# Kernel optimization log

Hardware: AMD Instinct MI355X
Metric: run time of the kernel (lower is better)

Reference implementation:

```python
import jax, jax.numpy as jnp
import numpy as np

N_NODES = 50000
N_EDGES = 1000000
D_IN = 128
HID = 64
N_GRAPHS = 256
NEG_SLOPE = 0.2


def _gatv2_layer(x, src, dst, Wl, Wr, att, b, n_nodes):
    # lin_l applied to source nodes, lin_r to target nodes (PyG GATv2Conv, heads=1)
    xl = x @ Wl.T  # [N, C]
    xr = x @ Wr.T  # [N, C]
    e = jax.nn.leaky_relu(xl[src] + xr[dst], NEG_SLOPE)  # [E, C]
    logits = e @ att  # [E]
    # segment softmax over destination node
    m = jax.ops.segment_max(logits, dst, num_segments=n_nodes)
    ex = jnp.exp(logits - m[dst])
    den = jax.ops.segment_sum(ex, dst, num_segments=n_nodes)
    alpha = ex / den[dst]  # [E]
    out = jax.ops.segment_sum(alpha[:, None] * xl[src], dst, num_segments=n_nodes)
    return out + b


def setup_inputs() -> dict:
    key = jax.random.key(0)
    ks = jax.random.split(key, 32)
    x = jax.random.normal(ks[0], (N_NODES, D_IN), dtype=jnp.float32)
    edge_index = jax.random.randint(ks[1], (2, N_EDGES), 0, N_NODES, dtype=jnp.int64)
    batch = jnp.sort(jax.random.randint(ks[2], (N_NODES,), 0, N_GRAPHS, dtype=jnp.int64))
    inp = {"x": x, "edge_index": edge_index, "batch": batch}
    dims = [D_IN, HID, HID]  # input dim per layer
    kidx = 3
    for i, din in enumerate(dims):
        inp[f"Wl{i}"] = jax.random.normal(ks[kidx], (HID, din), dtype=jnp.float32) * 0.1; kidx += 1
        inp[f"Wr{i}"] = jax.random.normal(ks[kidx], (HID, din), dtype=jnp.float32) * 0.1; kidx += 1
        inp[f"att{i}"] = jax.random.normal(ks[kidx], (HID,), dtype=jnp.float32) * 0.1; kidx += 1
        inp[f"b{i}"] = jnp.zeros((HID,), dtype=jnp.float32)
        inp[f"Rw{i}"] = jax.random.normal(ks[kidx], (HID, din), dtype=jnp.float32) * 0.1; kidx += 1
        inp[f"Rb{i}"] = jnp.zeros((HID,), dtype=jnp.float32)
    inp["Wf"] = jax.random.normal(ks[kidx], (1, HID), dtype=jnp.float32) * 0.1
    inp["bf"] = jnp.zeros((1,), dtype=jnp.float32)
    return inp


def reference(x, edge_index, batch, Wl0, Wr0, att0, b0, Rw0, Rb0,
              Wl1, Wr1, att1, b1, Rw1, Rb1,
              Wl2, Wr2, att2, b2, Rw2, Rb2, Wf, bf):
    n = x.shape[0]
    # add_self_loops=True (PyG default)
    loops = jnp.arange(n, dtype=edge_index.dtype)
    src = jnp.concatenate([edge_index[0], loops])
    dst = jnp.concatenate([edge_index[1], loops])
    layers = [(Wl0, Wr0, att0, b0, Rw0, Rb0),
              (Wl1, Wr1, att1, b1, Rw1, Rb1),
              (Wl2, Wr2, att2, b2, Rw2, Rb2)]
    for i, (Wl, Wr, att, b, Rw, Rb) in enumerate(layers):
        h = _gatv2_layer(x, src, dst, Wl, Wr, att, b, n) + (x @ Rw.T + Rb)  # res=True
        # norm=None -> Identity; dropout inactive at inference
        x = jax.nn.relu(h) if i < len(layers) - 1 else h
    # global_mean_pool
    sums = jax.ops.segment_sum(x, batch, num_segments=N_GRAPHS)
    cnt = jax.ops.segment_sum(jnp.ones((n,), x.dtype), batch, num_segments=N_GRAPHS)
    pooled = sums / jnp.maximum(cnt, 1.0)[:, None]
    return pooled @ Wf.T + bf
```

## Files before the change

kernel.cpp:

```cpp
#include <hip/hip_runtime.h>


#define NN 50000
#define NE 1000000
#define HID 64
#define DIN0 128
#define NG 256
#define NEG 0.2f

#define SCHUNK 1024
#define SNB ((NN + SCHUNK - 1) / SCHUNK)

typedef float f32x4 __attribute__((ext_vector_type(4)));
typedef short s8v __attribute__((ext_vector_type(8)));
typedef short s4v __attribute__((ext_vector_type(4)));
typedef __bf16 bf16x8 __attribute__((ext_vector_type(8)));
typedef _Float16 h2v __attribute__((ext_vector_type(2)));
typedef unsigned u32x2 __attribute__((ext_vector_type(2)));
typedef unsigned short u16;

__device__ __forceinline__ unsigned short f2bf(float f) {
    unsigned u = __float_as_uint(f);
    u = u + 0x7fffu + ((u >> 16) & 1u);
    return (unsigned short)(u >> 16);
}
__device__ __forceinline__ float bf2f(unsigned short v) {
    return __uint_as_float(((unsigned)v) << 16);
}
__device__ __forceinline__ short split_hi(float x) {
    return (short)f2bf(x);
}
__device__ __forceinline__ short split_lo(float x, short hi) {
    return (short)f2bf(x - bf2f((unsigned short)hi));
}
__device__ __forceinline__ h2v u2h(unsigned u) { return __builtin_bit_cast(h2v, u); }
__device__ __forceinline__ unsigned h2u(h2v h) { return __builtin_bit_cast(unsigned, h); }
__device__ __forceinline__ h2v pklo(unsigned a, unsigned b) {
    return u2h(__builtin_amdgcn_perm(b, a, 0x05040100u));
}
__device__ __forceinline__ h2v pkhi(unsigned a, unsigned b) {
    return u2h(__builtin_amdgcn_perm(b, a, 0x07060302u));
}
__device__ __forceinline__ float red32_add(float v) {
    unsigned u = __float_as_uint(v);
    u32x2 r = __builtin_amdgcn_permlane32_swap(u, u, false, false);
    return __uint_as_float(r[0]) + __uint_as_float(r[1]);
}
__device__ __forceinline__ float red32_max(float v) {
    unsigned u = __float_as_uint(v);
    u32x2 r = __builtin_amdgcn_permlane32_swap(u, u, false, false);
    return fmaxf(__uint_as_float(r[0]), __uint_as_float(r[1]));
}

__global__ __launch_bounds__(256) void k_wt_all(
        const float* __restrict__ Wl0, const float* __restrict__ Wr0, const float* __restrict__ Rw0,
        const float* __restrict__ Wl1, const float* __restrict__ Wr1, const float* __restrict__ Rw1,
        const float* __restrict__ Wl2, const float* __restrict__ Wr2, const float* __restrict__ Rw2,
        const float* __restrict__ att0, const float* __restrict__ att1, const float* __restrict__ att2,
        short* __restrict__ Ws0, short* __restrict__ Ws1, short* __restrict__ Ws2,
        _Float16* __restrict__ attp,
        int* __restrict__ startg, int* __restrict__ endg) {
    int i = blockIdx.x * 256 + threadIdx.x;
    if (i < 2 * NG) {
        if (i < NG) startg[i] = 0; else endg[i - NG] = 0;
    }
    if (i < 3 * HID) {
        int L = i >> 6, c = i & 63;
        const float* at = (L == 0) ? att0 : (L == 1) ? att1 : att2;
        float a = at[c];
        attp[L * 2 * HID + c] = (_Float16)(0.6f * a);
        attp[L * 2 * HID + HID + c] = (_Float16)(0.4f * a);
    }
    const int L0N = 3 * HID * DIN0;
    const int L1N = 3 * HID * HID;
    if (i >= L0N + 2 * L1N) return;
    const float* Wm; short* Ws; int din, local;
    if (i < L0N) {
        local = i; din = DIN0; Ws = Ws0;
        int m = local / (DIN0 * HID);
        Wm = (m == 0) ? Wl0 : (m == 1) ? Wr0 : Rw0;
    } else if (i < L0N + L1N) {
        local = i - L0N; din = HID; Ws = Ws1;
        int m = local / (HID * HID);
        Wm = (m == 0) ? Wl1 : (m == 1) ? Wr1 : Rw1;
    } else {
        local = i - L0N - L1N; din = HID; Ws = Ws2;
        int m = local / (HID * HID);
        Wm = (m == 0) ? Wl2 : (m == 1) ? Wr2 : Rw2;
    }
    int m = local / (din * HID);
    int r = local - m * (din * HID);
    int c = r / din, k = r - c * din;
    float w = Wm[c * din + k];
    short hi = split_hi(w);
    short lo = split_lo(w, hi);
    Ws[(((m * 2 + 0) * HID + c) * din) + k] = hi;
    Ws[(((m * 2 + 1) * HID + c) * din) + k] = lo;
}

__global__ void k_bounds(const int* __restrict__ batch,
                         int* __restrict__ startg, int* __restrict__ endg,
                         int* __restrict__ cnt8) {
    int i = blockIdx.x * 256 + threadIdx.x;
    if (i >= NN) return;
#pragma unroll
    for (int g = 0; g < 8; g++) cnt8[g * NN + i] = 0;
    int g = batch[i];
    if (i == 0 || batch[i - 1] != g) startg[g] = i;
    if (i == NN - 1 || batch[i + 1] != g) endg[g] = i + 1;
}

__global__ __launch_bounds__(256) void k_hist8(const int* __restrict__ edst,
                                               int* __restrict__ cnt8,
                                               u16* __restrict__ rank) {
    int* mycnt = cnt8 + (blockIdx.x & 7) * NN;
    for (int e = blockIdx.x * 256 + threadIdx.x; e < NE; e += 512 * 256) {
        int r = atomicAdd(&mycnt[edst[e]], 1);
        rank[e] = (u16)r;
    }
}

__global__ void k_hist_red(int* __restrict__ cnt8, int* __restrict__ cnt) {
    int i = blockIdx.x * 256 + threadIdx.x;
    if (i >= NN) return;
    int s = 1;
#pragma unroll
    for (int g = 0; g < 8; g++) {
        int t = cnt8[g * NN + i];
        cnt8[g * NN + i] = s;
        s += t;
    }
    cnt[i] = s;
}

__global__ __launch_bounds__(256) void k_scan_part(const int* __restrict__ cnt,
                                                   int* __restrict__ part) {
    __shared__ int ws[4];
    int b = blockIdx.x, t = threadIdx.x;
    int i0 = b * SCHUNK + t * 4;
    int s = 0;
#pragma unroll
    for (int j = 0; j < 4; j++) {
        int i = i0 + j;
        if (i < NN) s += cnt[i];
    }
#pragma unroll
    for (int o = 32; o; o >>= 1) s += __shfl_xor(s, o, 64);
    if ((t & 63) == 0) ws[t >> 6] = s;
    __syncthreads();
    if (t == 0) part[b] = ws[0] + ws[1] + ws[2] + ws[3];
}

__global__ void k_scan_small(const int* __restrict__ part, int* __restrict__ partScan) {
    __shared__ int sh[SNB];
    int t = threadIdx.x;
    if (t < SNB) sh[t] = part[t];
    __syncthreads();
    if (t < SNB) {
        int s = 0;
        for (int i = 0; i < t; i++) s += sh[i];
        partScan[t] = s;
    }
}

__global__ __launch_bounds__(256) void k_scan_emit(const int* __restrict__ cnt,
                                                   const int* __restrict__ partScan,
                                                   int* __restrict__ off,
                                                   u16* __restrict__ srcs) {
    __shared__ int tsum[256];
    int b = blockIdx.x, t = threadIdx.x;
    int i0 = b * SCHUNK + t * 4;
    int e[4], p[4];
    int s = 0;
#pragma unroll
    for (int j = 0; j < 4; j++) {
        int i = i0 + j;
        e[j] = (i < NN) ? cnt[i] : 0;
        p[j] = s;
        s += e[j];
    }
    tsum[t] = s;
    __syncthreads();
    for (int d = 1; d < 256; d <<= 1) {
        int v = (t >= d) ? tsum[t - d] : 0;
        __syncthreads();
        tsum[t] += v;
        __syncthreads();
    }
    int base = partScan[b] + ((t == 0) ? 0 : tsum[t - 1]);
#pragma unroll
    for (int j = 0; j < 4; j++) {
        int i = i0 + j;
        if (i < NN) {
            int v = base + p[j];
            off[i] = v;
            srcs[v] = (u16)i;
            if (i == NN - 1) off[NN] = v + e[j];
        }
    }
}

__global__ __launch_bounds__(256) void k_scatter_rank(
        const int* __restrict__ esrc, const int* __restrict__ edst,
        const int* __restrict__ off, const int* __restrict__ cnt8,
        const u16* __restrict__ rank, u16* __restrict__ srcs) {
    int e = blockIdx.x * 256 + threadIdx.x;
    if (e >= NE) return;
    int d = edst[e];
    int slice = (e >> 8) & 7;
    int pos = off[d] + cnt8[slice * NN + d] + (int)rank[e];
    srcs[pos] = (u16)esrc[e];
}

template <int DIN, bool RELU>
__global__ __launch_bounds__(256, 3) void k_gemm(
        const float* __restrict__ xin, const short* __restrict__ Ws,
        const float* __restrict__ bvec, const float* __restrict__ rb,
        _Float16* __restrict__ xl16, _Float16* __restrict__ xr16, float* __restrict__ acc) {
    constexpr int LROW = 40;
    __shared__ short lds[20480];
    short* xhi = lds;
    short* xlo = lds + 2560;

    const int tid = threadIdx.x;
    const int w = tid >> 6;
    const int lane = tid & 63;
    const int col = lane & 15;
    const int quad = lane >> 4;
    const int nb0 = blockIdx.x * 64;

    f32x4 d[3][4];
#pragma unroll
    for (int m = 0; m < 3; m++)
#pragma unroll
        for (int ct = 0; ct < 4; ct++) d[m][ct] = (f32x4){0.f, 0.f, 0.f, 0.f};

    for (int c0 = 0; c0 < DIN; c0 += 32) {
        if (c0) __syncthreads();
        for (int u = tid; u < 512; u += 256) {
            int row = u >> 3, kq = u & 7;
            int n = nb0 + row;
            float4 v = make_float4(0.f, 0.f, 0.f, 0.f);
            if (n < NN) {
                v = *(const float4*)&xin[(size_t)n * DIN + c0 + 4 * kq];
                if (RELU) {
                    v.x = fmaxf(v.x, 0.f); v.y = fmaxf(v.y, 0.f);
                    v.z = fmaxf(v.z, 0.f); v.w = fmaxf(v.w, 0.f);
                }
            }
            s4v h, l;
            short h0 = split_hi(v.x), l0 = split_lo(v.x, h0);
            short h1 = split_hi(v.y), l1 = split_lo(v.y, h1);
            short h2 = split_hi(v.z), l2 = split_lo(v.z, h2);
            short h3 = split_hi(v.w), l3 = split_lo(v.w, h3);
            h[0] = h0; h[1] = h1; h[2] = h2; h[3] = h3;
            l[0] = l0; l[1] = l1; l[2] = l2; l[3] = l3;
            *(s4v*)&xhi[row * LROW + 4 * kq] = h;
            *(s4v*)&xlo[row * LROW + 4 * kq] = l;
        }
        for (int u = tid; u < 1536; u += 256) {
            int mp = u >> 8;
            int r = u & 255;
            int c = r >> 2, q = r & 3;
            s8v v = *(const s8v*)&Ws[((mp * HID + c) * DIN) + c0 + 8 * q];
            *(s8v*)&lds[5120 + mp * 2560 + c * LROW + 8 * q] = v;
        }
        __syncthreads();

        bf16x8 a_h = __builtin_bit_cast(bf16x8,
            *(const s8v*)&xhi[(w * 16 + col) * LROW + quad * 8]);
        bf16x8 a_l = __builtin_bit_cast(bf16x8,
            *(const s8v*)&xlo[(w * 16 + col) * LROW + quad * 8]);

#pragma unroll
        for (int m = 0; m < 3; m++) {
#pragma unroll
            for (int ct = 0; ct < 4; ct++) {
                bf16x8 b_h = __builtin_bit_cast(bf16x8,
                    *(const s8v*)&lds[5120 + (m * 2 + 0) * 2560 + (ct * 16 + col) * LROW + quad * 8]);
                bf16x8 b_l = __builtin_bit_cast(bf16x8,
                    *(const s8v*)&lds[5120 + (m * 2 + 1) * 2560 + (ct * 16 + col) * LROW + quad * 8]);
                d[m][ct] = __builtin_amdgcn_mfma_f32_16x16x32_bf16(a_h, b_h, d[m][ct], 0, 0, 0);
                d[m][ct] = __builtin_amdgcn_mfma_f32_16x16x32_bf16(a_h, b_l, d[m][ct], 0, 0, 0);
                d[m][ct] = __builtin_amdgcn_mfma_f32_16x16x32_bf16(a_l, b_h, d[m][ct], 0, 0, 0);
            }
        }
    }

#pragma unroll
    for (int r = 0; r < 4; r++) {
        int n = nb0 + w * 16 + quad * 4 + r;
        if (n >= NN) continue;
        size_t base = (size_t)n * HID;
#pragma unroll
        for (int ct = 0; ct < 4; ct++) {
            int c = ct * 16 + col;
            xl16[base + c] = (_Float16)d[0][ct][r];
            xr16[base + c] = (_Float16)d[1][ct][r];
            acc[base + c] = d[2][ct][r] + bvec[c] + rb[c];
        }
    }
}

__global__ __launch_bounds__(256) void k_attn_dst(
        const int* __restrict__ off, const u16* __restrict__ srcs,
        const _Float16* __restrict__ xl16, const _Float16* __restrict__ xr16,
        const _Float16* __restrict__ attL, float* __restrict__ acc) {
    const int lane = threadIdx.x & 63;
    const int d = blockIdx.x * 4 + (threadIdx.x >> 6);
    if (d >= NN) return;
    const int e = lane >> 3;
    const int cg = lane & 7;

    const int lo = off[d], deg = off[d + 1] - lo;

    uint4 X = *(const uint4*)&xr16[(size_t)d * HID + 8 * cg];
    uint4 A6 = *(const uint4*)&attL[8 * cg];
    uint4 A4 = *(const uint4*)&attL[HID + 8 * cg];
    h2v xh0 = u2h(X.x), xh1 = u2h(X.y), xh2 = u2h(X.z), xh3 = u2h(X.w);
    h2v a60 = u2h(A6.x), a61 = u2h(A6.y), a62 = u2h(A6.z), a63 = u2h(A6.w);
    h2v a40 = u2h(A4.x), a41 = u2h(A4.y), a42 = u2h(A4.z), a43 = u2h(A4.w);

#define EDGE_LOGIT(S, U, T)                                                    \
    {                                                                          \
        U = *(const uint4*)&xl16[(size_t)(S) * HID + 8 * cg];                  \
        h2v _v; unsigned _a; float _ps;                                        \
        _v = u2h(U.x) + xh0; _a = h2u(_v) & 0x7FFF7FFFu;                       \
        _ps = __builtin_amdgcn_fdot2(a60, _v, 0.f, false);                     \
        _ps = __builtin_amdgcn_fdot2(a40, u2h(_a), _ps, false);                \
        _v = u2h(U.y) + xh1; _a = h2u(_v) & 0x7FFF7FFFu;                       \
        _ps = __builtin_amdgcn_fdot2(a61, _v, _ps, false);                     \
        _ps = __builtin_amdgcn_fdot2(a41, u2h(_a), _ps, false);                \
        _v = u2h(U.z) + xh2; _a = h2u(_v) & 0x7FFF7FFFu;                       \
        _ps = __builtin_amdgcn_fdot2(a62, _v, _ps, false);                     \
        _ps = __builtin_amdgcn_fdot2(a42, u2h(_a), _ps, false);                \
        _v = u2h(U.w) + xh3; _a = h2u(_v) & 0x7FFF7FFFu;                       \
        _ps = __builtin_amdgcn_fdot2(a63, _v, _ps, false);                     \
        _ps = __builtin_amdgcn_fdot2(a43, u2h(_a), _ps, false);                \
        _ps += __shfl_xor(_ps, 1, 64);                                         \
        _ps += __shfl_xor(_ps, 2, 64);                                         \
        _ps += __shfl_xor(_ps, 4, 64);                                         \
        T = _ps;                                                               \
    }

    float m = -INFINITY, l = 0.f;
    float4 oA = make_float4(0.f, 0.f, 0.f, 0.f);
    float4 oB = make_float4(0.f, 0.f, 0.f, 0.f);

    for (int base = 0; base < deg; base += 32) {
        const int rem = deg - base;
        int s0 = (int)srcs[lo + min(base + e, deg - 1)];
        int s1 = (int)srcs[lo + min(base + 8 + e, deg - 1)];

        uint4 U0, U1, U2, U3;
        float t0, t1, t2 = -INFINITY, t3 = -INFINITY;
        EDGE_LOGIT(s0, U0, t0);
        EDGE_LOGIT(s1, U1, t1);
        if (base + e >= deg) t0 = -INFINITY;
        if (base + 8 + e >= deg) t1 = -INFINITY;

        const bool do2 = rem > 16;
        if (do2) {
            int s2 = (int)srcs[lo + min(base + 16 + e, deg - 1)];
            EDGE_LOGIT(s2, U2, t2);
            if (base + 16 + e >= deg) t2 = -INFINITY;
            if (rem > 24) {
                int s3 = (int)srcs[lo + min(base + 24 + e, deg - 1)];
                EDGE_LOGIT(s3, U3, t3);
                if (base + 24 + e >= deg) t3 = -INFINITY;
            } else {
                U3 = U0;
            }
        }

        float cm = fmaxf(fmaxf(t0, t1), fmaxf(t2, t3));
        cm = fmaxf(cm, __shfl_xor(cm, 8, 64));
        cm = fmaxf(cm, __shfl_xor(cm, 16, 64));
        cm = red32_max(cm);
        if (cm > m) {
            float corr = __expf(m - cm);
            m = cm;
            l *= corr;
            oA.x *= corr; oA.y *= corr; oA.z *= corr; oA.w *= corr;
            oB.x *= corr; oB.y *= corr; oB.z *= corr; oB.w *= corr;
        }
        float p0 = __expf(t0 - m);
        float p1 = __expf(t1 - m);
        l += p0 + p1;
        h2v p01 = {(_Float16)p0, (_Float16)p1};
        oA.x = __builtin_amdgcn_fdot2(p01, pklo(U0.x, U1.x), oA.x, false);
        oA.y = __builtin_amdgcn_fdot2(p01, pkhi(U0.x, U1.x), oA.y, false);
        oA.z = __builtin_amdgcn_fdot2(p01, pklo(U0.y, U1.y), oA.z, false);
        oA.w = __builtin_amdgcn_fdot2(p01, pkhi(U0.y, U1.y), oA.w, false);
        oB.x = __builtin_amdgcn_fdot2(p01, pklo(U0.z, U1.z), oB.x, false);
        oB.y = __builtin_amdgcn_fdot2(p01, pkhi(U0.z, U1.z), oB.y, false);
        oB.z = __builtin_amdgcn_fdot2(p01, pklo(U0.w, U1.w), oB.z, false);
        oB.w = __builtin_amdgcn_fdot2(p01, pkhi(U0.w, U1.w), oB.w, false);
        if (do2) {
            float p2 = __expf(t2 - m);
            float p3 = __expf(t3 - m);
            l += p2 + p3;
            h2v p23 = {(_Float16)p2, (_Float16)p3};
            oA.x = __builtin_amdgcn_fdot2(p23, pklo(U2.x, U3.x), oA.x, false);
            oA.y = __builtin_amdgcn_fdot2(p23, pkhi(U2.x, U3.x), oA.y, false);
            oA.z = __builtin_amdgcn_fdot2(p23, pklo(U2.y, U3.y), oA.z, false);
            oA.w = __builtin_amdgcn_fdot2(p23, pkhi(U2.y, U3.y), oA.w, false);
            oB.x = __builtin_amdgcn_fdot2(p23, pklo(U2.z, U3.z), oB.x, false);
            oB.y = __builtin_amdgcn_fdot2(p23, pkhi(U2.z, U3.z), oB.y, false);
            oB.z = __builtin_amdgcn_fdot2(p23, pklo(U2.w, U3.w), oB.z, false);
            oB.w = __builtin_amdgcn_fdot2(p23, pkhi(U2.w, U3.w), oB.w, false);
        }
    }
#undef EDGE_LOGIT

#pragma unroll
    for (int w = 8; w <= 16; w <<= 1) {
        l    += __shfl_xor(l, w, 64);
        oA.x += __shfl_xor(oA.x, w, 64); oA.y += __shfl_xor(oA.y, w, 64);
        oA.z += __shfl_xor(oA.z, w, 64); oA.w += __shfl_xor(oA.w, w, 64);
        oB.x += __shfl_xor(oB.x, w, 64); oB.y += __shfl_xor(oB.y, w, 64);
        oB.z += __shfl_xor(oB.z, w, 64); oB.w += __shfl_xor(oB.w, w, 64);
    }
    l    = red32_add(l);
    oA.x = red32_add(oA.x); oA.y = red32_add(oA.y);
    oA.z = red32_add(oA.z); oA.w = red32_add(oA.w);
    oB.x = red32_add(oB.x); oB.y = red32_add(oB.y);
    oB.z = red32_add(oB.z); oB.w = red32_add(oB.w);

    if (e == 0) {
        float inv = 1.f / l;
        float4* a4 = (float4*)&acc[(size_t)d * HID + 8 * cg];
        float4 c0 = a4[0], c1 = a4[1];
        c0.x += oA.x * inv; c0.y += oA.y * inv;
        c0.z += oA.z * inv; c0.w += oA.w * inv;
        c1.x += oB.x * inv; c1.y += oB.y * inv;
        c1.z += oB.z * inv; c1.w += oB.w * inv;
        a4[0] = c0; a4[1] = c1;
    }
}

__global__ __launch_bounds__(512) void k_pool_final(
        const float* __restrict__ acc,
        const int* __restrict__ startg, const int* __restrict__ endg,
        const float* __restrict__ Wf, const float* __restrict__ bf_,
        float* __restrict__ out) {
    __shared__ float red[8][HID];
    const int g = blockIdx.x;
    const int c = threadIdx.x & 63;
    const int j = threadIdx.x >> 6;
    const int s = startg[g], epos = endg[g];

    float sum = 0.f;
    for (int n = s + j; n < epos; n += 8)
        sum += acc[(size_t)n * HID + c];
    red[j][c] = sum;
    __syncthreads();

    if (threadIdx.x < HID) {
        float tot = 0.f;
#pragma unroll
        for (int w = 0; w < 8; w++) tot += red[w][c];
        float cntf = (float)(epos - s);
        float v = tot / fmaxf(cntf, 1.f) * Wf[c];
#pragma unroll
        for (int o = 32; o; o >>= 1) v += __shfl_xor(v, o, 64);
        if (c == 0) out[g] = v + bf_[0];
    }
}

extern "C" void kernel_launch(void* const* d_in, const int* in_sizes, int n_in,
                              void* d_out, int out_size, void* d_ws, size_t ws_size,
                              hipStream_t stream) {
    const float* x   = (const float*)d_in[0];
    const int* eidx  = (const int*)d_in[1];
    const int* batch = (const int*)d_in[2];
    const int* esrc = eidx;
    const int* edst = eidx + NE;
    const float* Wf  = (const float*)d_in[21];
    const float* bfb = (const float*)d_in[22];

    float* wsf = (float*)d_ws;
    const size_t NN64 = (size_t)NN * HID;
    _Float16* xl16 = (_Float16*)wsf;
    _Float16* xr16 = (_Float16*)(wsf + NN64);
    float* acc0   = wsf + 2 * NN64;
    float* acc1   = acc0 + NN64;
    short* Ws0    = (short*)(acc1 + NN64);
    short* Ws1    = Ws0 + 2 * 3 * HID * DIN0;
    short* Ws2    = Ws1 + 2 * 3 * HID * HID;
    int*   ccnt   = (int*)(Ws2 + 2 * 3 * HID * HID);
    int*   startg = ccnt + NN;
    int*   endg   = startg + NG;
    int*   off    = endg + NG;
    int*   part   = off + NN + 1;
    int*   partSc = part + SNB;
    int*   cnt8   = partSc + SNB;
    u16*   rank   = (u16*)(cnt8 + 8 * NN);
    u16*   srcs   = rank + NE;
    _Float16* attp = (_Float16*)(srcs + NE + NN);

    k_wt_all<<<(3 * HID * DIN0 + 2 * 3 * HID * HID + 255) / 256, 256, 0, stream>>>(
        (const float*)d_in[3], (const float*)d_in[4], (const float*)d_in[7],
        (const float*)d_in[9], (const float*)d_in[10], (const float*)d_in[13],
        (const float*)d_in[15], (const float*)d_in[16], (const float*)d_in[19],
        (const float*)d_in[5], (const float*)d_in[11], (const float*)d_in[17],
        Ws0, Ws1, Ws2, attp, startg, endg);
    k_bounds<<<(NN + 255) / 256, 256, 0, stream>>>(batch, startg, endg, cnt8);

    k_hist8<<<512, 256, 0, stream>>>(edst, cnt8, rank);
    k_hist_red<<<(NN + 255) / 256, 256, 0, stream>>>(cnt8, ccnt);
    k_scan_part<<<SNB, 256, 0, stream>>>(ccnt, part);
    k_scan_small<<<1, 64, 0, stream>>>(part, partSc);
    k_scan_emit<<<SNB, 256, 0, stream>>>(ccnt, partSc, off, srcs);
    k_scatter_rank<<<(NE + 255) / 256, 256, 0, stream>>>(esrc, edst, off, cnt8, rank, srcs);

    const short* Wss[3] = {Ws0, Ws1, Ws2};
    float* accs[4] = {acc0, acc0, acc1, acc0};
    const int gemm_grid = (NN + 63) / 64;
    for (int L = 0; L < 3; L++) {
        const float* b   = (const float*)d_in[3 + L * 6 + 3];
        const float* Rb  = (const float*)d_in[3 + L * 6 + 5];
        float* accOut = accs[L + 1];

        if (L == 0)
            k_gemm<DIN0, false><<<gemm_grid, 256, 0, stream>>>(
                x, Wss[0], b, Rb, xl16, xr16, accOut);
        else
            k_gemm<HID, true><<<gemm_grid, 256, 0, stream>>>(
                accs[L], Wss[L], b, Rb, xl16, xr16, accOut);

        k_attn_dst<<<(NN + 3) / 4, 256, 0, stream>>>(
            off, srcs, xl16, xr16, attp + L * 2 * HID, accOut);
    }

    k_pool_final<<<NG, 512, 0, stream>>>(accs[3], startg, endg, Wf, bfb, (float*)d_out);
}
```

Before: 347.3 us.

## Fuse preprocessing kernels and use DPP/swizzle reductions in attention

Merges weight split and batch-bounds into one prep kernel, folds the histogram reduction into the scan-partial kernel, and replaces the single-block partial scan with a per-block wave reduction, cutting three kernel launches. In the attention kernel, the octet and cross-octet reductions use DPP and ds_swizzle in place of generic shuffles, dot products use two independent accumulators, and all source indices are loaded up front. This reduces launch overhead and cross-lane reduction latency, at the cost of more register pressure and redundant source loads for low-degree nodes.

```diff
diff --git a/kernel.cpp b/kernel.cpp
--- a/kernel.cpp
+++ b/kernel.cpp
@@ -41,6 +41,15 @@
 __device__ __forceinline__ h2v pkhi(unsigned a, unsigned b) {
     return u2h(__builtin_amdgcn_perm(b, a, 0x07060302u));
 }
+template <int CTRL>
+__device__ __forceinline__ float dpp_mv(float v) {
+    return __int_as_float(
+        __builtin_amdgcn_update_dpp(0, __float_as_int(v), CTRL, 0xF, 0xF, true));
+}
+template <int OFF>
+__device__ __forceinline__ float swz(float v) {
+    return __int_as_float(__builtin_amdgcn_ds_swizzle(__float_as_int(v), OFF));
+}
 __device__ __forceinline__ float red32_add(float v) {
     unsigned u = __float_as_uint(v);
     u32x2 r = __builtin_amdgcn_permlane32_swap(u, u, false, false);
@@ -51,25 +60,58 @@
     u32x2 r = __builtin_amdgcn_permlane32_swap(u, u, false, false);
     return fmaxf(__uint_as_float(r[0]), __uint_as_float(r[1]));
 }
-
-__global__ __launch_bounds__(256) void k_wt_all(
+__device__ __forceinline__ float octet_sum(float v) {
+    v += dpp_mv<0xB1>(v);
+    v += dpp_mv<0x4E>(v);
+    v += swz<0x101F>(v);
+    return v;
+}
+__device__ __forceinline__ float esum(float v) {
+    v += dpp_mv<0x128>(v);
+    v += swz<0x401F>(v);
+    return red32_add(v);
+}
+__device__ __forceinline__ float emax(float v) {
+    v = fmaxf(v, dpp_mv<0x128>(v));
+    v = fmaxf(v, swz<0x401F>(v));
+    return red32_max(v);
+}
+
+__global__ __launch_bounds__(256) void k_prep(
         const float* __restrict__ Wl0, const float* __restrict__ Wr0, const float* __restrict__ Rw0,
         const float* __restrict__ Wl1, const float* __restrict__ Wr1, const float* __restrict__ Rw1,
         const float* __restrict__ Wl2, const float* __restrict__ Wr2, const float* __restrict__ Rw2,
         const float* __restrict__ att0, const float* __restrict__ att1, const float* __restrict__ att2,
         short* __restrict__ Ws0, short* __restrict__ Ws1, short* __restrict__ Ws2,
         _Float16* __restrict__ attp,
-        int* __restrict__ startg, int* __restrict__ endg) {
+        const int* __restrict__ batch,
+        int* __restrict__ startg, int* __restrict__ endg,
+        int* __restrict__ cnt8) {
     int i = blockIdx.x * 256 + threadIdx.x;
-    if (i < 2 * NG) {
-        if (i < NG) startg[i] = 0; else endg[i - NG] = 0;
-    }
     if (i < 3 * HID) {
         int L = i >> 6, c = i & 63;
         const float* at = (L == 0) ? att0 : (L == 1) ? att1 : att2;
         float a = at[c];
         attp[L * 2 * HID + c] = (_Float16)(0.6f * a);
         attp[L * 2 * HID + HID + c] = (_Float16)(0.4f * a);
+    }
+    if (i < NN) {
+#pragma unroll
+        for (int g = 0; g < 8; g++) cnt8[g * NN + i] = 0;
+        int g = batch[i];
+        if (i == 0) {
+            startg[g] = 0;
+            for (int g2 = 0; g2 < g; g2++) { startg[g2] = 0; endg[g2] = 0; }
+        } else if (batch[i - 1] != g) {
+            startg[g] = i;
+            for (int g2 = batch[i - 1] + 1; g2 < g; g2++) { startg[g2] = i; endg[g2] = i; }
+        }
+        if (i == NN - 1) {
+            endg[g] = NN;
+            for (int g2 = g + 1; g2 < NG; g2++) { startg[g2] = NN; endg[g2] = NN; }
+        } else if (batch[i + 1] != g) {
+            endg[g] = i + 1;
+        }
     }
     const int L0N = 3 * HID * DIN0;
     const int L1N = 3 * HID * HID;
@@ -98,18 +140,6 @@
     Ws[(((m * 2 + 1) * HID + c) * din) + k] = lo;
 }
 
-__global__ void k_bounds(const int* __restrict__ batch,
-                         int* __restrict__ startg, int* __restrict__ endg,
-                         int* __restrict__ cnt8) {
-    int i = blockIdx.x * 256 + threadIdx.x;
-    if (i >= NN) return;
-#pragma unroll
-    for (int g = 0; g < 8; g++) cnt8[g * NN + i] = 0;
-    int g = batch[i];
-    if (i == 0 || batch[i - 1] != g) startg[g] = i;
-    if (i == NN - 1 || batch[i + 1] != g) endg[g] = i + 1;
-}
-
 __global__ __launch_bounds__(256) void k_hist8(const int* __restrict__ edst,
                                                int* __restrict__ cnt8,
                                                u16* __restrict__ rank) {
@@ -120,55 +150,48 @@
     }
 }
 
-__global__ void k_hist_red(int* __restrict__ cnt8, int* __restrict__ cnt) {
-    int i = blockIdx.x * 256 + threadIdx.x;
-    if (i >= NN) return;
-    int s = 1;
-#pragma unroll
-    for (int g = 0; g < 8; g++) {
-        int t = cnt8[g * NN + i];
-        cnt8[g * NN + i] = s;
-        s += t;
-    }
-    cnt[i] = s;
-}
-
-__global__ __launch_bounds__(256) void k_scan_part(const int* __restrict__ cnt,
-                                                   int* __restrict__ part) {
+__global__ __launch_bounds__(256) void k_histscan(int* __restrict__ cnt8,
+                                                  int* __restrict__ cnt,
+                                                  int* __restrict__ part) {
     __shared__ int ws[4];
     int b = blockIdx.x, t = threadIdx.x;
     int i0 = b * SCHUNK + t * 4;
-    int s = 0;
+    int tot = 0;
 #pragma unroll
     for (int j = 0; j < 4; j++) {
         int i = i0 + j;
-        if (i < NN) s += cnt[i];
-    }
-#pragma unroll
-    for (int o = 32; o; o >>= 1) s += __shfl_xor(s, o, 64);
-    if ((t & 63) == 0) ws[t >> 6] = s;
+        if (i < NN) {
+            int s = 1;
+#pragma unroll
+            for (int g = 0; g < 8; g++) {
+                int v = cnt8[g * NN + i];
+                cnt8[g * NN + i] = s;
+                s += v;
+            }
+            cnt[i] = s;
+            tot += s;
+        }
+    }
+#pragma unroll
+    for (int o = 32; o; o >>= 1) tot += __shfl_xor(tot, o, 64);
+    if ((t & 63) == 0) ws[t >> 6] = tot;
     __syncthreads();
     if (t == 0) part[b] = ws[0] + ws[1] + ws[2] + ws[3];
 }
 
-__global__ void k_scan_small(const int* __restrict__ part, int* __restrict__ partScan) {
-    __shared__ int sh[SNB];
-    int t = threadIdx.x;
-    if (t < SNB) sh[t] = part[t];
-    __syncthreads();
-    if (t < SNB) {
-        int s = 0;
-        for (int i = 0; i < t; i++) s += sh[i];
-        partScan[t] = s;
-    }
-}
-
 __global__ __launch_bounds__(256) void k_scan_emit(const int* __restrict__ cnt,
-                                                   const int* __restrict__ partScan,
+                                                   const int* __restrict__ part,
                                                    int* __restrict__ off,
                                                    u16* __restrict__ srcs) {
     __shared__ int tsum[256];
+    __shared__ int baseSh;
     int b = blockIdx.x, t = threadIdx.x;
+    if (t < 64) {
+        int v = (t < b && t < SNB) ? part[t] : 0;
+#pragma unroll
+        for (int o = 32; o; o >>= 1) v += __shfl_xor(v, o, 64);
+        if (t == 0) baseSh = v;
+    }
     int i0 = b * SCHUNK + t * 4;
     int e[4], p[4];
     int s = 0;
@@ -187,7 +210,7 @@
         tsum[t] += v;
         __syncthreads();
     }
-    int base = partScan[b] + ((t == 0) ? 0 : tsum[t - 1]);
+    int base = baseSh + ((t == 0) ? 0 : tsum[t - 1]);
 #pragma unroll
     for (int j = 0; j < 4; j++) {
         int i = i0 + j;
@@ -321,26 +344,23 @@
     h2v a60 = u2h(A6.x), a61 = u2h(A6.y), a62 = u2h(A6.z), a63 = u2h(A6.w);
     h2v a40 = u2h(A4.x), a41 = u2h(A4.y), a42 = u2h(A4.z), a43 = u2h(A4.w);
 
-#define EDGE_LOGIT(S, U, T)                                                    \
+#define EDGE_DOT(S, U, PS)                                                     \
     {                                                                          \
         U = *(const uint4*)&xl16[(size_t)(S) * HID + 8 * cg];                  \
-        h2v _v; unsigned _a; float _ps;                                        \
+        h2v _v; unsigned _a; float _q0, _q1;                                   \
         _v = u2h(U.x) + xh0; _a = h2u(_v) & 0x7FFF7FFFu;                       \
-        _ps = __builtin_amdgcn_fdot2(a60, _v, 0.f, false);                     \
-        _ps = __builtin_amdgcn_fdot2(a40, u2h(_a), _ps, false);                \
+        _q0 = __builtin_amdgcn_fdot2(a60, _v, 0.f, false);                     \
+        _q1 = __builtin_amdgcn_fdot2(a40, u2h(_a), 0.f, false);                \
         _v = u2h(U.y) + xh1; _a = h2u(_v) & 0x7FFF7FFFu;                       \
-        _ps = __builtin_amdgcn_fdot2(a61, _v, _ps, false);                     \
-        _ps = __builtin_amdgcn_fdot2(a41, u2h(_a), _ps, false);                \
+        _q0 = __builtin_amdgcn_fdot2(a61, _v, _q0, false);                     \
+        _q1 = __builtin_amdgcn_fdot2(a41, u2h(_a), _q1, false);                \
         _v = u2h(U.z) + xh2; _a = h2u(_v) & 0x7FFF7FFFu;                       \
-        _ps = __builtin_amdgcn_fdot2(a62, _v, _ps, false);                     \
-        _ps = __builtin_amdgcn_fdot2(a42, u2h(_a), _ps, false);                \
+        _q0 = __builtin_amdgcn_fdot2(a62, _v, _q0, false);                     \
+        _q1 = __builtin_amdgcn_fdot2(a42, u2h(_a), _q1, false);                \
         _v = u2h(U.w) + xh3; _a = h2u(_v) & 0x7FFF7FFFu;                       \
-        _ps = __builtin_amdgcn_fdot2(a63, _v, _ps, false);                     \
-        _ps = __builtin_amdgcn_fdot2(a43, u2h(_a), _ps, false);                \
-        _ps += __shfl_xor(_ps, 1, 64);                                         \
-        _ps += __shfl_xor(_ps, 2, 64);                                         \
-        _ps += __shfl_xor(_ps, 4, 64);                                         \
-        T = _ps;                                                               \
+        _q0 = __builtin_amdgcn_fdot2(a63, _v, _q0, false);                     \
+        _q1 = __builtin_amdgcn_fdot2(a43, u2h(_a), _q1, false);                \
+        PS = _q0 + _q1;                                                        \
     }
 
     float m = -INFINITY, l = 0.f;
@@ -351,32 +371,34 @@
         const int rem = deg - base;
         int s0 = (int)srcs[lo + min(base + e, deg - 1)];
         int s1 = (int)srcs[lo + min(base + 8 + e, deg - 1)];
+        int s2 = (int)srcs[lo + min(base + 16 + e, deg - 1)];
+        int s3 = (int)srcs[lo + min(base + 24 + e, deg - 1)];
 
         uint4 U0, U1, U2, U3;
+        float ps0, ps1, ps2, ps3;
         float t0, t1, t2 = -INFINITY, t3 = -INFINITY;
-        EDGE_LOGIT(s0, U0, t0);
-        EDGE_LOGIT(s1, U1, t1);
+        EDGE_DOT(s0, U0, ps0);
+        EDGE_DOT(s1, U1, ps1);
+        t0 = octet_sum(ps0);
+        t1 = octet_sum(ps1);
         if (base + e >= deg) t0 = -INFINITY;
         if (base + 8 + e >= deg) t1 = -INFINITY;
 
         const bool do2 = rem > 16;
         if (do2) {
-            int s2 = (int)srcs[lo + min(base + 16 + e, deg - 1)];
-            EDGE_LOGIT(s2, U2, t2);
+            EDGE_DOT(s2, U2, ps2);
+            t2 = octet_sum(ps2);
             if (base + 16 + e >= deg) t2 = -INFINITY;
             if (rem > 24) {
-                int s3 = (int)srcs[lo + min(base + 24 + e, deg - 1)];
-                EDGE_LOGIT(s3, U3, t3);
+                EDGE_DOT(s3, U3, ps3);
+                t3 = octet_sum(ps3);
                 if (base + 24 + e >= deg) t3 = -INFINITY;
             } else {
                 U3 = U0;
             }
         }
 
-        float cm = fmaxf(fmaxf(t0, t1), fmaxf(t2, t3));
-        cm = fmaxf(cm, __shfl_xor(cm, 8, 64));
-        cm = fmaxf(cm, __shfl_xor(cm, 16, 64));
-        cm = red32_max(cm);
+        float cm = emax(fmaxf(fmaxf(t0, t1), fmaxf(t2, t3)));
         if (cm > m) {
             float corr = __expf(m - cm);
             m = cm;
@@ -411,21 +433,13 @@
             oB.w = __builtin_amdgcn_fdot2(p23, pkhi(U2.w, U3.w), oB.w, false);
         }
     }
-#undef EDGE_LOGIT
-
-#pragma unroll
-    for (int w = 8; w <= 16; w <<= 1) {
-        l    += __shfl_xor(l, w, 64);
-        oA.x += __shfl_xor(oA.x, w, 64); oA.y += __shfl_xor(oA.y, w, 64);
-        oA.z += __shfl_xor(oA.z, w, 64); oA.w += __shfl_xor(oA.w, w, 64);
-        oB.x += __shfl_xor(oB.x, w, 64); oB.y += __shfl_xor(oB.y, w, 64);
-        oB.z += __shfl_xor(oB.z, w, 64); oB.w += __shfl_xor(oB.w, w, 64);
-    }
-    l    = red32_add(l);
-    oA.x = red32_add(oA.x); oA.y = red32_add(oA.y);
-    oA.z = red32_add(oA.z); oA.w = red32_add(oA.w);
-    oB.x = red32_add(oB.x); oB.y = red32_add(oB.y);
-    oB.z = red32_add(oB.z); oB.w = red32_add(oB.w);
+#undef EDGE_DOT
+
+    l    = esum(l);
+    oA.x = esum(oA.x); oA.y = esum(oA.y);
+    oA.z = esum(oA.z); oA.w = esum(oA.w);
+    oB.x = esum(oB.x); oB.y = esum(oB.y);
+    oB.z = esum(oB.z); oB.w = esum(oB.w);
 
     if (e == 0) {
         float inv = 1.f / l;
@@ -499,19 +513,16 @@
     u16*   srcs   = rank + NE;
     _Float16* attp = (_Float16*)(srcs + NE + NN);
 
-    k_wt_all<<<(3 * HID * DIN0 + 2 * 3 * HID * HID + 255) / 256, 256, 0, stream>>>(
+    k_prep<<<(NN + 255) / 256, 256, 0, stream>>>(
         (const float*)d_in[3], (const float*)d_in[4], (const float*)d_in[7],
         (const float*)d_in[9], (const float*)d_in[10], (const float*)d_in[13],
         (const float*)d_in[15], (const float*)d_in[16], (const float*)d_in[19],
         (const float*)d_in[5], (const float*)d_in[11], (const float*)d_in[17],
-        Ws0, Ws1, Ws2, attp, startg, endg);
-    k_bounds<<<(NN + 255) / 256, 256, 0, stream>>>(batch, startg, endg, cnt8);
+        Ws0, Ws1, Ws2, attp, batch, startg, endg, cnt8);
 
     k_hist8<<<512, 256, 0, stream>>>(edst, cnt8, rank);
-    k_hist_red<<<(NN + 255) / 256, 256, 0, stream>>>(cnt8, ccnt);
-    k_scan_part<<<SNB, 256, 0, stream>>>(ccnt, part);
-    k_scan_small<<<1, 64, 0, stream>>>(part, partSc);
-    k_scan_emit<<<SNB, 256, 0, stream>>>(ccnt, partSc, off, srcs);
+    k_histscan<<<SNB, 256, 0, stream>>>(cnt8, ccnt, part);
+    k_scan_emit<<<SNB, 256, 0, stream>>>(ccnt, part, off, srcs);
     k_scatter_rank<<<(NE + 255) / 256, 256, 0, stream>>>(esrc, edst, off, cnt8, rank, srcs);
 
     const short* Wss[3] = {Ws0, Ws1, Ws2};
```

Result: faster. 325.7 us (-6.2%).
